# Kernel optimization log

Hardware: AMD Instinct MI355X
Metric: run time of the kernel (lower is better)

## Reference

```python
import jax, jax.numpy as jnp
import numpy as np

L, N, D_IN = 4, 2048, 1024
H, DH = 8, 64
INNER = H * DH          # 512
D_OUT = D_IN            # out_dim defaults to input_dim
SCALE = DH ** -0.5


def setup_inputs() -> dict:
    key = jax.random.key(0)
    ks = jax.random.split(key, 7)
    x = jax.random.normal(ks[0], (L, N, D_IN), jnp.float32)
    # torch Linear weights are [out_features, in_features]; xavier-ish scale
    Wq = jax.random.normal(ks[1], (INNER, D_IN), jnp.float32) * 0.03
    Wk = jax.random.normal(ks[2], (INNER, D_IN), jnp.float32) * 0.03
    Wv = jax.random.normal(ks[3], (INNER, D_IN), jnp.float32) * 0.03
    Wo = jax.random.normal(ks[4], (D_OUT, INNER), jnp.float32) * 0.03
    bo = jnp.zeros((D_OUT,), jnp.float32)
    # boolean key-padding mask [L, n]; ensure at least one valid key per row
    mask = jax.random.uniform(ks[5], (L, N)) < 0.9
    mask = mask.at[:, 0].set(True)
    return {"x": x, "Wq": Wq, "Wk": Wk, "Wv": Wv, "Wo": Wo, "bo": bo, "mask": mask}


def reference(x, Wq, Wk, Wv, Wo, bo, mask):
    # projections (Linear: y = x @ W^T), split heads: L n (h d) -> l h n d
    def split_heads(t):
        return t.reshape(L, N, H, DH).transpose(0, 2, 1, 3)

    q = split_heads(jnp.einsum('lnd,ed->lne', x, Wq))
    k = split_heads(jnp.einsum('lnd,ed->lne', x, Wk))  # context defaults to x
    v = split_heads(jnp.einsum('lnd,ed->lne', x, Wv))

    sim = jnp.einsum('lhnd,lhmd->lhnm', q, k) * SCALE   # [L,H,N,N]
    neg = -jnp.finfo(sim.dtype).max
    sim = jnp.where(mask[:, None, None, :], sim, neg)   # mask over key dim
    attn = jax.nn.softmax(sim, axis=-1)

    out = jnp.einsum('lhnm,lhmd->lhnd', attn, v)        # [L,H,N,DH]
    out = out.transpose(0, 2, 1, 3).reshape(L, N, INNER)
    return out @ Wo.T + bo                               # [L,N,D_OUT]
```

## Files before the change

### kernel.cpp

```cpp
#include <hip/hip_runtime.h>
#include <hip/hip_bf16.h>

#define L_DIM 4
#define N_DIM 2048
#define DIN   1024
#define H_DIM 8
#define DH    64
#define INNER 512

typedef __attribute__((ext_vector_type(8))) short short8;
typedef __attribute__((ext_vector_type(4))) float f32x4;

__device__ __forceinline__ unsigned short f2bf(float f) {
  unsigned u = __builtin_bit_cast(unsigned, f);
  u += 0x7fffu + ((u >> 16) & 1u);
  return (unsigned short)(u >> 16);
}

__device__ __forceinline__ unsigned cvtpk(float a, float b) {
  unsigned r;
  asm("v_cvt_pk_bf16_f32 %0, %1, %2" : "=v"(r) : "v"(a), "v"(b));
  return r;
}

__device__ __forceinline__ float fexp2(float x) {
  float r;
  asm("v_exp_f32 %0, %1" : "=v"(r) : "v"(x));
  return r;
}

typedef __attribute__((address_space(3))) unsigned int lds_uint;
typedef const __attribute__((address_space(1))) unsigned int glob_uint;
__device__ __forceinline__ void gl_lds16(const unsigned short* g,
                                         unsigned short* l) {
  __builtin_amdgcn_global_load_lds((glob_uint*)g, (lds_uint*)l, 16, 0, 0);
}

__global__ void cast_all(const float* __restrict__ x,
                         const float* __restrict__ wq,
                         const float* __restrict__ wk,
                         const float* __restrict__ wv,
                         const float* __restrict__ wo,
                         unsigned short* __restrict__ xb,
                         unsigned short* __restrict__ w3,
                         unsigned short* __restrict__ wob,
                         const unsigned char* __restrict__ mraw,
                         float* __restrict__ bias) {
  __shared__ int votes[2];
  int bid = blockIdx.x, t = threadIdx.x;
  if (bid == 10240) {
    if (t < 2) votes[t] = 0;
    __syncthreads();
    const unsigned int* m32 = (const unsigned int*)mraw;
    int anyf = 0, any8 = 0;
    for (int i = t; i < 2048; i += 256) {
      unsigned w = m32[i];
      if (w == 0x3f800000u) anyf = 1;
      if (w & 0xffffff00u) any8 = 1;
    }
    if (anyf) atomicOr(&votes[0], 1);
    if (any8) atomicOr(&votes[1], 1);
    __syncthreads();
    int fmt = votes[0] ? 2 : (votes[1] ? 1 : 0);
    for (int i = t; i < L_DIM * N_DIM; i += 256) {
      int mv;
      if (fmt == 2)      mv = ((const float*)mraw)[i] != 0.0f;
      else if (fmt == 1) mv = mraw[i] != 0;
      else               mv = ((const int*)mraw)[i] != 0;
      bias[i] = mv ? 0.0f : -1e30f;
    }
    return;
  }
  int i = (bid * 256 + t) * 4;
  const float* src; unsigned short* dst; int off;
  if (i < 8388608)      { src = x;  dst = xb;           off = i; }
  else if (i < 8912896) { src = wq; dst = w3;           off = i - 8388608; }
  else if (i < 9437184) { src = wk; dst = w3 + 524288;  off = i - 8912896; }
  else if (i < 9961472) { src = wv; dst = w3 + 1048576; off = i - 9437184; }
  else                  { src = wo; dst = wob;          off = i - 9961472; }
  float4 f = *(const float4*)(src + off);
  ushort4 o4;
  o4.x = f2bf(f.x); o4.y = f2bf(f.y); o4.z = f2bf(f.z); o4.w = f2bf(f.w);
  *(ushort4*)(dst + off) = o4;
}

__launch_bounds__(256, 3)
__global__ void gemm_qkv(const unsigned short* __restrict__ xb,
                         const unsigned short* __restrict__ w3,
                         unsigned short* __restrict__ qp,
                         unsigned short* __restrict__ kp,
                         unsigned short* __restrict__ vtp) {
  __shared__ __align__(16) unsigned short Sh[16384];
  const int tid = threadIdx.x, lane = tid & 63, wid = tid >> 6;
  const int l16 = lane & 15, quad = lane >> 4;
  const int wm = wid >> 1, wn = wid & 1;
  const int m0 = blockIdx.x * 128, n0 = blockIdx.y * 128;

  int aoff[2], boff[2], lofs[2];
#pragma unroll
  for (int it = 0; it < 2; ++it) {
    int c = it * 256 + wid * 64 + lane;
    int row = c >> 2, kseg = c & 3;
    aoff[it] = (m0 + row) * DIN + kseg * 8;
    boff[it] = (n0 + row) * DIN + kseg * 8;
    lofs[it] = (it * 256 + wid * 64) * 8;
  }

#pragma unroll
  for (int it = 0; it < 2; ++it) {
    gl_lds16(&xb[aoff[it]], &Sh[lofs[it]]);
    gl_lds16(&w3[boff[it]], &Sh[8192 + lofs[it]]);
  }

  f32x4 acc[4][4] = {};
  for (int t = 0; t < 32; ++t) {
    const int buf = t & 1;
    __syncthreads();
    if (t < 31) {
      int kt2 = (t + 1) * 32, b2 = buf ^ 1;
#pragma unroll
      for (int it = 0; it < 2; ++it) {
        gl_lds16(&xb[aoff[it] + kt2], &Sh[b2 * 4096 + lofs[it]]);
        gl_lds16(&w3[boff[it] + kt2], &Sh[8192 + b2 * 4096 + lofs[it]]);
      }
    }
    const unsigned short* As = &Sh[buf * 4096];
    const unsigned short* Bs = &Sh[8192 + buf * 4096];
    short8 af[4], bf[4];
#pragma unroll
    for (int mt = 0; mt < 4; ++mt)
      af[mt] = *(const short8*)&As[(wm * 64 + mt * 16 + l16) * 32 + quad * 8];
#pragma unroll
    for (int nt = 0; nt < 4; ++nt)
      bf[nt] = *(const short8*)&Bs[(wn * 64 + nt * 16 + l16) * 32 + quad * 8];
#pragma unroll
    for (int mt = 0; mt < 4; ++mt)
#pragma unroll
      for (int nt = 0; nt < 4; ++nt)
        acc[mt][nt] = __builtin_amdgcn_mfma_f32_16x16x32_bf16(
            af[mt], bf[nt], acc[mt][nt], 0, 0, 0);
  }
  if (blockIdx.y >= 8) {
    const int l = m0 >> 11, mloc = m0 & 2047;
#pragma unroll
    for (int chunk = 0; chunk < 2; ++chunk) {
      __syncthreads();
      if (wn == chunk) {
#pragma unroll
        for (int mt = 0; mt < 4; ++mt)
#pragma unroll
          for (int nt = 0; nt < 4; ++nt) {
            int col = nt * 16 + l16;
            int rowb = wm * 64 + mt * 16 + quad * 4;
            ushort4 pv;
            pv.x = f2bf(acc[mt][nt][0]);
            pv.y = f2bf(acc[mt][nt][1]);
            pv.z = f2bf(acc[mt][nt][2]);
            pv.w = f2bf(acc[mt][nt][3]);
            *(ushort4*)&Sh[col * 136 + rowb] = pv;
          }
      }
      __syncthreads();
      int hh = ((n0 + chunk * 64) & 511) >> 6;
#pragma unroll
      for (int it = 0; it < 4; ++it) {
        int c = it * 256 + tid;
        int cl = c >> 4, seg = c & 15;
        short8 vv = *(const short8*)&Sh[cl * 136 + seg * 8];
        *(short8*)&vtp[((size_t)((l * H_DIM + hh) * DH + cl)) * N_DIM + mloc +
                       seg * 8] = vv;
      }
    }
  } else {
#pragma unroll
    for (int mt = 0; mt < 4; ++mt)
#pragma unroll
      for (int nt = 0; nt < 4; ++nt)
#pragma unroll
        for (int r = 0; r < 4; ++r) {
          int grow = m0 + wm * 64 + mt * 16 + quad * 4 + r;
          int gcol = n0 + wn * 64 + nt * 16 + l16;
          unsigned short bv = f2bf(acc[mt][nt][r]);
          int h = (gcol & 511) >> 6, d = gcol & 63;
          int l = grow >> 11, n = grow & 2047;
          unsigned short* dst = (gcol >> 9) ? kp : qp;
          dst[(((l * H_DIM + h) * N_DIM + n) * DH) + d] = bv;
        }
  }
}

#define PW_S 64
__launch_bounds__(128, 2)
__global__ void attn_kernel(const unsigned short* __restrict__ qg,
                            const unsigned short* __restrict__ kg,
                            const unsigned short* __restrict__ vtg,
                            const float* __restrict__ bias,
                            unsigned short* __restrict__ aout) {
  __shared__ __align__(16) unsigned short Ks[2][64 * 64];
  __shared__ __align__(16) unsigned short Vs[2][64 * 64];
  __shared__ __align__(16) unsigned short Pw[64 * PW_S];
  const int tid = threadIdx.x, lane = tid & 63, wid = tid >> 6;
  const int l16 = lane & 15, quad = lane >> 4;
  const int bid = blockIdx.x;
  const int xcd = bid & 7, j = bid >> 3;
  const int lh = xcd * 4 + (j >> 5);
  const int q0 = (j & 31) << 6;
  const int l = lh >> 3, h = lh & 7;
  const unsigned short* Qb = qg + (size_t)lh * N_DIM * DH;
  const unsigned short* Kb = kg + (size_t)lh * N_DIM * DH;
  const unsigned short* Vt = vtg + (size_t)lh * DH * N_DIM;
  const float* bl = bias + l * N_DIM;

  short8 qf[2][2];
#pragma unroll
  for (int mt = 0; mt < 2; ++mt)
#pragma unroll
    for (int ks = 0; ks < 2; ++ks)
      qf[mt][ks] = *(const short8*)&Qb[(q0 + wid * 32 + mt * 16 + l16) * DH +
                                       ks * 32 + quad * 8];

  f32x4 o[2][4] = {};
  float lsum[2] = {0.f, 0.f};

  int kof[4], ldsb[4];
  size_t vof[4];
#pragma unroll
  for (int it = 0; it < 4; ++it) {
    int cb = it * 128 + wid * 64, c = cb + lane;
    int rr = c >> 3, sl = c & 7, gs = (sl + rr) & 7;
    kof[it] = rr * DH + gs * 8;
    vof[it] = (size_t)rr * N_DIM + gs * 8;
    ldsb[it] = cb * 8;
  }

#pragma unroll
  for (int it = 0; it < 4; ++it) {
    gl_lds16(&Kb[kof[it]], &Ks[0][ldsb[it]]);
    gl_lds16(&Vt[vof[it]], &Vs[0][ldsb[it]]);
  }

  for (int t = 0; t < 32; ++t) {
    const int kv = t << 6, buf = t & 1;
    __syncthreads();
    if (t < 31) {
      int kv2 = kv + 64, b2 = buf ^ 1;
#pragma unroll
      for (int it = 0; it < 4; ++it) {
        gl_lds16(&Kb[(kv2 << 6) + kof[it]], &Ks[b2][ldsb[it]]);
        gl_lds16(&Vt[vof[it] + kv2], &Vs[b2][ldsb[it]]);
      }
    }
    const unsigned short* Kst = Ks[buf];
    const unsigned short* Vst = Vs[buf];

    f32x4 sc[2][4] = {};
#pragma unroll
    for (int nt = 0; nt < 4; ++nt)
#pragma unroll
      for (int ks = 0; ks < 2; ++ks) {
        int s = (ks * 4 + quad - l16) & 7;
        short8 kf = *(const short8*)&Kst[(nt * 16 + l16) * 64 + s * 8];
#pragma unroll
        for (int mt = 0; mt < 2; ++mt)
          sc[mt][nt] = __builtin_amdgcn_mfma_f32_16x16x32_bf16(
              kf, qf[mt][ks], sc[mt][nt], 0, 0, 0);
      }
#pragma unroll
    for (int mt = 0; mt < 2; ++mt) {
      unsigned short* pr = &Pw[(wid * 32 + mt * 16 + l16) * PW_S];
#pragma unroll
      for (int nt = 0; nt < 4; ++nt) {
        float4 b4 = *(const float4*)&bl[kv + nt * 16 + quad * 4];
        float p0 = fexp2(fmaf(sc[mt][nt][0], 0.18033688011f, b4.x));
        float p1 = fexp2(fmaf(sc[mt][nt][1], 0.18033688011f, b4.y));
        float p2 = fexp2(fmaf(sc[mt][nt][2], 0.18033688011f, b4.z));
        float p3 = fexp2(fmaf(sc[mt][nt][3], 0.18033688011f, b4.w));
        lsum[mt] += (p0 + p1) + (p2 + p3);
        uint2 pk = make_uint2(cvtpk(p0, p1), cvtpk(p2, p3));
        int gk = nt * 2 + (quad >> 1);
        int s = (gk + l16) & 7;
        *(uint2*)&pr[s * 8 + (quad & 1) * 4] = pk;
      }
    }
#pragma unroll
    for (int g = 0; g < 2; ++g) {
      short8 pa[2];
#pragma unroll
      for (int mt = 0; mt < 2; ++mt) {
        int sp = (g * 4 + quad + l16) & 7;
        pa[mt] = *(const short8*)&Pw[(wid * 32 + mt * 16 + l16) * PW_S +
                                     sp * 8];
      }
#pragma unroll
      for (int nt = 0; nt < 4; ++nt) {
        int dd = nt * 16 + l16;
        int sv2 = (g * 4 + quad - l16) & 7;
        short8 vb = *(const short8*)&Vst[dd * 64 + sv2 * 8];
#pragma unroll
        for (int mt = 0; mt < 2; ++mt)
          o[mt][nt] = __builtin_amdgcn_mfma_f32_16x16x32_bf16(
              pa[mt], vb, o[mt][nt], 0, 0, 0);
      }
    }
  }
#pragma unroll
  for (int mt = 0; mt < 2; ++mt) {
    lsum[mt] += __shfl_xor(lsum[mt], 16);
    lsum[mt] += __shfl_xor(lsum[mt], 32);
  }
#pragma unroll
  for (int mt = 0; mt < 2; ++mt)
#pragma unroll
    for (int r = 0; r < 4; ++r) {
      float inv = 1.f / __shfl(lsum[mt], quad * 4 + r);
      int row = q0 + wid * 32 + mt * 16 + quad * 4 + r;
#pragma unroll
      for (int nt = 0; nt < 4; ++nt)
        aout[(size_t)(l * N_DIM + row) * INNER + h * DH + nt * 16 + l16] =
            f2bf(o[mt][nt][r] * inv);
    }
}

__launch_bounds__(256, 3)
__global__ void gemm_out(const unsigned short* __restrict__ a,
                         const unsigned short* __restrict__ wo,
                         const float* __restrict__ bo,
                         float* __restrict__ out) {
  __shared__ __align__(16) unsigned short Sh[16384];
  const int tid = threadIdx.x, lane = tid & 63, wid = tid >> 6;
  const int l16 = lane & 15, quad = lane >> 4;
  const int wm = wid >> 1, wn = wid & 1;
  const int m0 = blockIdx.x * 128, n0 = blockIdx.y * 128;

  int aoff[2], boff[2], lofs[2];
#pragma unroll
  for (int it = 0; it < 2; ++it) {
    int c = it * 256 + wid * 64 + lane;
    int row = c >> 2, kseg = c & 3;
    aoff[it] = (m0 + row) * INNER + kseg * 8;
    boff[it] = (n0 + row) * INNER + kseg * 8;
    lofs[it] = (it * 256 + wid * 64) * 8;
  }

#pragma unroll
  for (int it = 0; it < 2; ++it) {
    gl_lds16(&a[aoff[it]], &Sh[lofs[it]]);
    gl_lds16(&wo[boff[it]], &Sh[8192 + lofs[it]]);
  }

  f32x4 acc[4][4] = {};
  for (int t = 0; t < 16; ++t) {
    const int buf = t & 1;
    __syncthreads();
    if (t < 15) {
      int kt2 = (t + 1) * 32, b2 = buf ^ 1;
#pragma unroll
      for (int it = 0; it < 2; ++it) {
        gl_lds16(&a[aoff[it] + kt2], &Sh[b2 * 4096 + lofs[it]]);
        gl_lds16(&wo[boff[it] + kt2], &Sh[8192 + b2 * 4096 + lofs[it]]);
      }
    }
    const unsigned short* As = &Sh[buf * 4096];
    const unsigned short* Bs = &Sh[8192 + buf * 4096];
    short8 af[4], bf[4];
#pragma unroll
    for (int mt = 0; mt < 4; ++mt)
      af[mt] = *(const short8*)&As[(wm * 64 + mt * 16 + l16) * 32 + quad * 8];
#pragma unroll
    for (int nt = 0; nt < 4; ++nt)
      bf[nt] = *(const short8*)&Bs[(wn * 64 + nt * 16 + l16) * 32 + quad * 8];
#pragma unroll
    for (int mt = 0; mt < 4; ++mt)
#pragma unroll
      for (int nt = 0; nt < 4; ++nt)
        acc[mt][nt] = __builtin_amdgcn_mfma_f32_16x16x32_bf16(
            af[mt], bf[nt], acc[mt][nt], 0, 0, 0);
  }
#pragma unroll
  for (int mt = 0; mt < 4; ++mt)
#pragma unroll
    for (int nt = 0; nt < 4; ++nt)
#pragma unroll
      for (int r = 0; r < 4; ++r) {
        int grow = m0 + wm * 64 + mt * 16 + quad * 4 + r;
        int gcol = n0 + wn * 64 + nt * 16 + l16;
        out[(size_t)grow * DIN + gcol] = acc[mt][nt][r] + bo[gcol];
      }
}

extern "C" void kernel_launch(void* const* d_in, const int* in_sizes, int n_in,
                              void* d_out, int out_size, void* d_ws,
                              size_t ws_size, hipStream_t stream) {
  const float* x  = (const float*)d_in[0];
  const float* Wq = (const float*)d_in[1];
  const float* Wk = (const float*)d_in[2];
  const float* Wv = (const float*)d_in[3];
  const float* Wo = (const float*)d_in[4];
  const float* bo = (const float*)d_in[5];
  const unsigned char* mask = (const unsigned char*)d_in[6];
  float* out = (float*)d_out;

  char* ws = (char*)d_ws;
  unsigned short* xb  = (unsigned short*)(ws + 0);
  unsigned short* w3  = (unsigned short*)(ws + 16777216);
  unsigned short* wob = (unsigned short*)(ws + 19922944);
  unsigned short* q   = (unsigned short*)(ws + 20971520);
  unsigned short* k   = (unsigned short*)(ws + 29360128);
  unsigned short* vt  = (unsigned short*)(ws + 37748736);
  unsigned short* att = (unsigned short*)(ws + 46137344);
  float* bias         = (float*)(ws + 54525952);

  cast_all<<<10241, 256, 0, stream>>>(x, Wq, Wk, Wv, Wo, xb, w3, wob, mask,
                                      bias);
  gemm_qkv<<<dim3(64, 12), 256, 0, stream>>>(xb, w3, q, k, vt);
  attn_kernel<<<1024, 128, 0, stream>>>(q, k, vt, bias, att);
  gemm_out<<<dim3(64, 8), 256, 0, stream>>>(att, wob, bo, out);
}
```

Before: 215.1 us.

## Use 32x32x16 MFMA in attention and keep P in registers instead of LDS

The attention kernel moves from 16x16x32 to 32x32x16 bf16 MFMAs, computing S^T so that each lane's softmax outputs already form the A-operand layout for the PV product. This removes the Pw shared-memory round trip and its LDS reads and writes. It also adds s_setprio around the MFMA sections so wavefronts favour matrix-instruction issue. V operands are now assembled from two 8-byte LDS reads, which adds LDS instructions, and the larger accumulators may raise register pressure.

```diff
diff --git a/kernel.cpp b/kernel.cpp
--- a/kernel.cpp
+++ b/kernel.cpp
@@ -10,6 +10,7 @@
 
 typedef __attribute__((ext_vector_type(8))) short short8;
 typedef __attribute__((ext_vector_type(4))) float f32x4;
+typedef __attribute__((ext_vector_type(16))) float f32x16;
 
 __device__ __forceinline__ unsigned short f2bf(float f) {
   unsigned u = __builtin_bit_cast(unsigned, f);
@@ -189,7 +190,6 @@
   }
 }
 
-#define PW_S 64
 __launch_bounds__(128, 2)
 __global__ void attn_kernel(const unsigned short* __restrict__ qg,
                             const unsigned short* __restrict__ kg,
@@ -198,9 +198,8 @@
                             unsigned short* __restrict__ aout) {
   __shared__ __align__(16) unsigned short Ks[2][64 * 64];
   __shared__ __align__(16) unsigned short Vs[2][64 * 64];
-  __shared__ __align__(16) unsigned short Pw[64 * PW_S];
   const int tid = threadIdx.x, lane = tid & 63, wid = tid >> 6;
-  const int l16 = lane & 15, quad = lane >> 4;
+  const int l32 = lane & 31, hi = lane >> 5;
   const int bid = blockIdx.x;
   const int xcd = bid & 7, j = bid >> 3;
   const int lh = xcd * 4 + (j >> 5);
@@ -211,16 +210,14 @@
   const unsigned short* Vt = vtg + (size_t)lh * DH * N_DIM;
   const float* bl = bias + l * N_DIM;
 
-  short8 qf[2][2];
-#pragma unroll
-  for (int mt = 0; mt < 2; ++mt)
-#pragma unroll
-    for (int ks = 0; ks < 2; ++ks)
-      qf[mt][ks] = *(const short8*)&Qb[(q0 + wid * 32 + mt * 16 + l16) * DH +
-                                       ks * 32 + quad * 8];
-
-  f32x4 o[2][4] = {};
-  float lsum[2] = {0.f, 0.f};
+  short8 qf[4];
+#pragma unroll
+  for (int ks = 0; ks < 4; ++ks)
+    qf[ks] = *(const short8*)&Qb[(q0 + wid * 32 + l32) * DH + ks * 16 +
+                                 hi * 8];
+
+  f32x16 o[2] = {};
+  float lsum = 0.f;
 
   int kof[4], ldsb[4];
   size_t vof[4];
@@ -253,71 +250,72 @@
     const unsigned short* Kst = Ks[buf];
     const unsigned short* Vst = Vs[buf];
 
-    f32x4 sc[2][4] = {};
-#pragma unroll
-    for (int nt = 0; nt < 4; ++nt)
-#pragma unroll
-      for (int ks = 0; ks < 2; ++ks) {
-        int s = (ks * 4 + quad - l16) & 7;
-        short8 kf = *(const short8*)&Kst[(nt * 16 + l16) * 64 + s * 8];
-#pragma unroll
-        for (int mt = 0; mt < 2; ++mt)
-          sc[mt][nt] = __builtin_amdgcn_mfma_f32_16x16x32_bf16(
-              kf, qf[mt][ks], sc[mt][nt], 0, 0, 0);
-      }
-#pragma unroll
-    for (int mt = 0; mt < 2; ++mt) {
-      unsigned short* pr = &Pw[(wid * 32 + mt * 16 + l16) * PW_S];
-#pragma unroll
-      for (int nt = 0; nt < 4; ++nt) {
-        float4 b4 = *(const float4*)&bl[kv + nt * 16 + quad * 4];
-        float p0 = fexp2(fmaf(sc[mt][nt][0], 0.18033688011f, b4.x));
-        float p1 = fexp2(fmaf(sc[mt][nt][1], 0.18033688011f, b4.y));
-        float p2 = fexp2(fmaf(sc[mt][nt][2], 0.18033688011f, b4.z));
-        float p3 = fexp2(fmaf(sc[mt][nt][3], 0.18033688011f, b4.w));
-        lsum[mt] += (p0 + p1) + (p2 + p3);
-        uint2 pk = make_uint2(cvtpk(p0, p1), cvtpk(p2, p3));
-        int gk = nt * 2 + (quad >> 1);
-        int s = (gk + l16) & 7;
-        *(uint2*)&pr[s * 8 + (quad & 1) * 4] = pk;
-      }
-    }
-#pragma unroll
-    for (int g = 0; g < 2; ++g) {
-      short8 pa[2];
+    f32x16 sc[2] = {};
+    __builtin_amdgcn_s_setprio(1);
+#pragma unroll
+    for (int ks = 0; ks < 4; ++ks) {
+      int cg = ks * 2 + hi;
 #pragma unroll
       for (int mt = 0; mt < 2; ++mt) {
-        int sp = (g * 4 + quad + l16) & 7;
-        pa[mt] = *(const short8*)&Pw[(wid * 32 + mt * 16 + l16) * PW_S +
-                                     sp * 8];
-      }
-#pragma unroll
-      for (int nt = 0; nt < 4; ++nt) {
-        int dd = nt * 16 + l16;
-        int sv2 = (g * 4 + quad - l16) & 7;
-        short8 vb = *(const short8*)&Vst[dd * 64 + sv2 * 8];
-#pragma unroll
-        for (int mt = 0; mt < 2; ++mt)
-          o[mt][nt] = __builtin_amdgcn_mfma_f32_16x16x32_bf16(
-              pa[mt], vb, o[mt][nt], 0, 0, 0);
-      }
-    }
-  }
-#pragma unroll
-  for (int mt = 0; mt < 2; ++mt) {
-    lsum[mt] += __shfl_xor(lsum[mt], 16);
-    lsum[mt] += __shfl_xor(lsum[mt], 32);
-  }
-#pragma unroll
-  for (int mt = 0; mt < 2; ++mt)
-#pragma unroll
-    for (int r = 0; r < 4; ++r) {
-      float inv = 1.f / __shfl(lsum[mt], quad * 4 + r);
-      int row = q0 + wid * 32 + mt * 16 + quad * 4 + r;
-#pragma unroll
-      for (int nt = 0; nt < 4; ++nt)
-        aout[(size_t)(l * N_DIM + row) * INNER + h * DH + nt * 16 + l16] =
-            f2bf(o[mt][nt][r] * inv);
+        int key = mt * 32 + l32;
+        short8 kf =
+            *(const short8*)&Kst[key * 64 + ((cg - key) & 7) * 8];
+        sc[mt] = __builtin_amdgcn_mfma_f32_32x32x16_bf16(kf, qf[ks], sc[mt],
+                                                         0, 0, 0);
+      }
+    }
+    __builtin_amdgcn_s_setprio(0);
+
+    unsigned pk[2][4][2];
+#pragma unroll
+    for (int mt = 0; mt < 2; ++mt)
+#pragma unroll
+      for (int rg = 0; rg < 4; ++rg) {
+        float4 b4 = *(const float4*)&bl[kv + mt * 32 + rg * 8 + hi * 4];
+        float p0 = fexp2(fmaf(sc[mt][rg * 4 + 0], 0.18033688011f, b4.x));
+        float p1 = fexp2(fmaf(sc[mt][rg * 4 + 1], 0.18033688011f, b4.y));
+        float p2 = fexp2(fmaf(sc[mt][rg * 4 + 2], 0.18033688011f, b4.z));
+        float p3 = fexp2(fmaf(sc[mt][rg * 4 + 3], 0.18033688011f, b4.w));
+        lsum += (p0 + p1) + (p2 + p3);
+        pk[mt][rg][0] = cvtpk(p0, p1);
+        pk[mt][rg][1] = cvtpk(p2, p3);
+      }
+
+    __builtin_amdgcn_s_setprio(1);
+#pragma unroll
+    for (int ks = 0; ks < 4; ++ks) {
+      int mt = ks >> 1, s = ks & 1;
+      short8 pa = __builtin_bit_cast(
+          short8, make_uint4(pk[mt][s * 2][0], pk[mt][s * 2][1],
+                             pk[mt][s * 2 + 1][0], pk[mt][s * 2 + 1][1]));
+#pragma unroll
+      for (int nt = 0; nt < 2; ++nt) {
+        int d = nt * 32 + l32;
+        const unsigned short* vr = &Vst[d * 64 + hi * 4];
+        uint2 v0 = *(const uint2*)&vr[(((ks * 2) - d) & 7) * 8];
+        uint2 v1 = *(const uint2*)&vr[(((ks * 2 + 1) - d) & 7) * 8];
+        short8 vb =
+            __builtin_bit_cast(short8, make_uint4(v0.x, v0.y, v1.x, v1.y));
+        o[nt] = __builtin_amdgcn_mfma_f32_32x32x16_bf16(pa, vb, o[nt],
+                                                        0, 0, 0);
+      }
+    }
+    __builtin_amdgcn_s_setprio(0);
+  }
+
+  lsum += __shfl_xor(lsum, 32);
+  float inv = 1.f / lsum;
+  const int rbase = l * N_DIM + q0 + wid * 32;
+#pragma unroll
+  for (int rg = 0; rg < 4; ++rg)
+#pragma unroll
+    for (int jj = 0; jj < 4; ++jj) {
+      int row = rg * 8 + hi * 4 + jj;
+      float invr = __shfl(inv, row);
+#pragma unroll
+      for (int nt = 0; nt < 2; ++nt)
+        aout[(size_t)(rbase + row) * INNER + h * DH + nt * 32 + l32] =
+            f2bf(o[nt][rg * 4 + jj] * invr);
     }
 }
 
```

New measurement: 217.6 us. Within noise of the previous version (+1.1%).

## Stage Q/K epilogue through LDS for coalesced stores; shrink out-GEMM N tile

Applied to the files above, without the earlier changes.

In the QKV GEMM, the Q/K epilogue now writes bf16 accumulators into shared memory one 64-column head chunk at a time, then each thread writes 16-byte vectors to the head-major Q/K layout. This replaces the scattered 2-byte global stores. Separately, the output GEMM tile drops from 128x128 to 128x64, doubling the grid to 1024 blocks and raising the occupancy hint to 4. This adds two extra barriers per chunk in the epilogue, and the smaller out tile reloads the A operand more often from global memory.

```diff
diff --git a/kernel.cpp b/kernel.cpp
--- a/kernel.cpp
+++ b/kernel.cpp
@@ -172,20 +172,36 @@
       }
     }
   } else {
-#pragma unroll
-    for (int mt = 0; mt < 4; ++mt)
-#pragma unroll
-      for (int nt = 0; nt < 4; ++nt)
-#pragma unroll
-        for (int r = 0; r < 4; ++r) {
-          int grow = m0 + wm * 64 + mt * 16 + quad * 4 + r;
-          int gcol = n0 + wn * 64 + nt * 16 + l16;
-          unsigned short bv = f2bf(acc[mt][nt][r]);
-          int h = (gcol & 511) >> 6, d = gcol & 63;
-          int l = grow >> 11, n = grow & 2047;
-          unsigned short* dst = (gcol >> 9) ? kp : qp;
-          dst[(((l * H_DIM + h) * N_DIM + n) * DH) + d] = bv;
-        }
+    const int l = m0 >> 11, nloc = m0 & 2047;
+    const int hbase = (n0 & 511) >> 6;
+    unsigned short* dstp = (n0 >> 9) ? kp : qp;
+#pragma unroll
+    for (int chunk = 0; chunk < 2; ++chunk) {
+      __syncthreads();
+      if (wn == chunk) {
+#pragma unroll
+        for (int mt = 0; mt < 4; ++mt)
+#pragma unroll
+          for (int nt = 0; nt < 4; ++nt) {
+            int col = nt * 16 + l16;
+            int rowb = wm * 64 + mt * 16 + quad * 4;
+#pragma unroll
+            for (int r = 0; r < 4; ++r)
+              Sh[(rowb + r) * 72 + col] = f2bf(acc[mt][nt][r]);
+          }
+      }
+      __syncthreads();
+      int hh = hbase + chunk;
+      unsigned short* db =
+          dstp + ((size_t)(l * H_DIM + hh) * N_DIM + nloc) * DH;
+#pragma unroll
+      for (int it = 0; it < 4; ++it) {
+        int c = it * 256 + tid;
+        int row = c >> 3, seg = c & 7;
+        short8 vv = *(const short8*)&Sh[row * 72 + seg * 8];
+        *(short8*)&db[row * DH + seg * 8] = vv;
+      }
+    }
   }
 }
 
@@ -321,69 +337,73 @@
     }
 }
 
-__launch_bounds__(256, 3)
+__launch_bounds__(256, 4)
 __global__ void gemm_out(const unsigned short* __restrict__ a,
                          const unsigned short* __restrict__ wo,
                          const float* __restrict__ bo,
                          float* __restrict__ out) {
-  __shared__ __align__(16) unsigned short Sh[16384];
+  __shared__ __align__(16) unsigned short Sh[12288];
   const int tid = threadIdx.x, lane = tid & 63, wid = tid >> 6;
   const int l16 = lane & 15, quad = lane >> 4;
   const int wm = wid >> 1, wn = wid & 1;
-  const int m0 = blockIdx.x * 128, n0 = blockIdx.y * 128;
-
-  int aoff[2], boff[2], lofs[2];
+  const int m0 = blockIdx.x * 128, n0 = blockIdx.y * 64;
+
+  int aoff[2], lofsA[2];
 #pragma unroll
   for (int it = 0; it < 2; ++it) {
     int c = it * 256 + wid * 64 + lane;
     int row = c >> 2, kseg = c & 3;
     aoff[it] = (m0 + row) * INNER + kseg * 8;
-    boff[it] = (n0 + row) * INNER + kseg * 8;
-    lofs[it] = (it * 256 + wid * 64) * 8;
-  }
-
-#pragma unroll
-  for (int it = 0; it < 2; ++it) {
-    gl_lds16(&a[aoff[it]], &Sh[lofs[it]]);
-    gl_lds16(&wo[boff[it]], &Sh[8192 + lofs[it]]);
-  }
-
-  f32x4 acc[4][4] = {};
+    lofsA[it] = (it * 256 + wid * 64) * 8;
+  }
+  int boff, lofsB;
+  {
+    int c = wid * 64 + lane;
+    int row = c >> 2, kseg = c & 3;
+    boff = (n0 + row) * INNER + kseg * 8;
+    lofsB = (wid * 64) * 8;
+  }
+
+#pragma unroll
+  for (int it = 0; it < 2; ++it)
+    gl_lds16(&a[aoff[it]], &Sh[lofsA[it]]);
+  gl_lds16(&wo[boff], &Sh[8192 + lofsB]);
+
+  f32x4 acc[4][2] = {};
   for (int t = 0; t < 16; ++t) {
     const int buf = t & 1;
     __syncthreads();
     if (t < 15) {
       int kt2 = (t + 1) * 32, b2 = buf ^ 1;
 #pragma unroll
-      for (int it = 0; it < 2; ++it) {
-        gl_lds16(&a[aoff[it] + kt2], &Sh[b2 * 4096 + lofs[it]]);
-        gl_lds16(&wo[boff[it] + kt2], &Sh[8192 + b2 * 4096 + lofs[it]]);
-      }
+      for (int it = 0; it < 2; ++it)
+        gl_lds16(&a[aoff[it] + kt2], &Sh[b2 * 4096 + lofsA[it]]);
+      gl_lds16(&wo[boff + kt2], &Sh[8192 + b2 * 2048 + lofsB]);
     }
     const unsigned short* As = &Sh[buf * 4096];
-    const unsigned short* Bs = &Sh[8192 + buf * 4096];
-    short8 af[4], bf[4];
+    const unsigned short* Bs = &Sh[8192 + buf * 2048];
+    short8 af[4], bf[2];
 #pragma unroll
     for (int mt = 0; mt < 4; ++mt)
       af[mt] = *(const short8*)&As[(wm * 64 + mt * 16 + l16) * 32 + quad * 8];
 #pragma unroll
-    for (int nt = 0; nt < 4; ++nt)
-      bf[nt] = *(const short8*)&Bs[(wn * 64 + nt * 16 + l16) * 32 + quad * 8];
+    for (int nt = 0; nt < 2; ++nt)
+      bf[nt] = *(const short8*)&Bs[(wn * 32 + nt * 16 + l16) * 32 + quad * 8];
 #pragma unroll
     for (int mt = 0; mt < 4; ++mt)
 #pragma unroll
-      for (int nt = 0; nt < 4; ++nt)
+      for (int nt = 0; nt < 2; ++nt)
         acc[mt][nt] = __builtin_amdgcn_mfma_f32_16x16x32_bf16(
             af[mt], bf[nt], acc[mt][nt], 0, 0, 0);
   }
 #pragma unroll
   for (int mt = 0; mt < 4; ++mt)
 #pragma unroll
-    for (int nt = 0; nt < 4; ++nt)
+    for (int nt = 0; nt < 2; ++nt)
 #pragma unroll
       for (int r = 0; r < 4; ++r) {
         int grow = m0 + wm * 64 + mt * 16 + quad * 4 + r;
-        int gcol = n0 + wn * 64 + nt * 16 + l16;
+        int gcol = n0 + wn * 32 + nt * 16 + l16;
         out[(size_t)grow * DIN + gcol] = acc[mt][nt][r] + bo[gcol];
       }
 }
@@ -414,5 +434,5 @@
                                       bias);
   gemm_qkv<<<dim3(64, 12), 256, 0, stream>>>(xb, w3, q, k, vt);
   attn_kernel<<<1024, 128, 0, stream>>>(q, k, vt, bias, att);
-  gemm_out<<<dim3(64, 8), 256, 0, stream>>>(att, wob, bo, out);
-}
+  gemm_out<<<dim3(64, 16), 256, 0, stream>>>(att, wob, bo, out);
+}
```

After: 218.0 us. About the same (+1.3%).
